# Optimization experiments

Measured on AMD Instinct MI355X. Metric: run time of the kernel, lower is better.

The kernel has to match this reference:

```python
import jax, jax.numpy as jnp
import numpy as np

N, F_IN, H, C, E = 50000, 512, 128, 64, 800000


def setup_inputs() -> dict:
    key = jax.random.key(0)
    ks = jax.random.split(key, 20)
    stdv = 1.0 / np.sqrt(H)
    std_att = 1.0
    std_att_vec = 1.0 / np.sqrt(3.0)
    u = lambda k, shape, s: jax.random.uniform(k, shape, jnp.float32, -s, s)
    inp = {
        "x": jax.random.normal(ks[0], (N, F_IN), jnp.float32),
        "edge_row": jax.random.randint(ks[1], (E,), 0, N, jnp.int32),
        "edge_col": jax.random.randint(ks[2], (E,), 0, N, jnp.int32),
        "edge_val": jax.random.uniform(ks[3], (E,), jnp.float32) * (1.0 / 16.0),
        "weight_low": u(ks[4], (F_IN, H), stdv),
        "weight_high": u(ks[5], (F_IN, H), stdv),
        "weight_mlp": u(ks[6], (F_IN, H), stdv),
        "att_vec_low": u(ks[7], (H, 1), std_att),
        "att_vec_high": u(ks[8], (H, 1), std_att),
        "att_vec_mlp": u(ks[9], (H, 1), std_att),
        "att_vec": u(ks[10], (3, 3), std_att_vec),
        "weight_low2": u(ks[11], (H, C), stdv),
        "weight_high2": u(ks[12], (H, C), stdv),
        "weight_mlp2": u(ks[13], (H, C), stdv),
        "att_vec_low2": u(ks[14], (C, 1), std_att),
        "att_vec_high2": u(ks[15], (C, 1), std_att),
        "att_vec_mlp2": u(ks[16], (C, 1), std_att),
        "att_vec2": u(ks[17], (3, 3), std_att_vec),
    }
    return inp


def _spmm_low(row, col, val, X):
    # adj_low @ X via gather + segment-sum over edges
    return jax.ops.segment_sum(val[:, None] * X[col], row, num_segments=N)


def _attention(o_low, o_high, o_mlp, a_low, a_high, a_mlp, a_vec):
    T = 3.0
    feats = jnp.concatenate([o_low @ a_low, o_high @ a_high, o_mlp @ a_mlp], axis=1)  # [N,3]
    att = jax.nn.softmax(jax.nn.sigmoid(feats) @ a_vec / T, axis=1)
    return att[:, 0:1], att[:, 1:2], att[:, 2:3]


def _layer(X, row, col, val, W_l, W_h, W_m, a_l, a_h, a_m, a_vec):
    xl = X @ W_l
    xh = X @ W_h
    o_low = jax.nn.relu(_spmm_low(row, col, val, xl))
    o_high = jax.nn.relu(xh - _spmm_low(row, col, val, xh))  # (I - adj_low) @ xh
    o_mlp = jax.nn.relu(X @ W_m)
    al, ah, am = _attention(o_low, o_high, o_mlp, a_l, a_h, a_m, a_vec)
    return 3.0 * (al * o_low + ah * o_high + am * o_mlp)


def reference(x, edge_row, edge_col, edge_val, weight_low, weight_high, weight_mlp,
              att_vec_low, att_vec_high, att_vec_mlp, att_vec,
              weight_low2, weight_high2, weight_mlp2,
              att_vec_low2, att_vec_high2, att_vec_mlp2, att_vec2):
    h = _layer(x, edge_row, edge_col, edge_val, weight_low, weight_high, weight_mlp,
               att_vec_low, att_vec_high, att_vec_mlp, att_vec)
    out = _layer(h, edge_row, edge_col, edge_val, weight_low2, weight_high2, weight_mlp2,
                 att_vec_low2, att_vec_high2, att_vec_mlp2, att_vec2)
    return jax.nn.log_softmax(out, axis=1)
```

## Files before the change

### kernel.cpp

```cpp
#include <hip/hip_runtime.h>
#include <hip/hip_bf16.h>

#define NN 50000
#define F_IN 512
#define HH 128
#define CC 64

typedef __attribute__((ext_vector_type(8))) short short8v;
typedef __attribute__((ext_vector_type(4))) float f32x4;
typedef __attribute__((ext_vector_type(2))) float f32x2;

__device__ __forceinline__ short f2b(float f) {
    unsigned u = __builtin_bit_cast(unsigned, f);
    unsigned r = (u + 0x7fffu + ((u >> 16) & 1u)) >> 16;
    return (short)r;
}
__device__ __forceinline__ float b2f(short s) {
    unsigned u = ((unsigned)(unsigned short)s) << 16;
    return __builtin_bit_cast(float, u);
}
__device__ __forceinline__ float b2f_lo(unsigned p) {
    return __builtin_bit_cast(float, p << 16);
}
__device__ __forceinline__ float b2f_hi(unsigned p) {
    return __builtin_bit_cast(float, p & 0xffff0000u);
}

__device__ __forceinline__ f32x2 q2_lo(unsigned p) {
    return __builtin_amdgcn_cvt_pk_f32_fp8(p, false);
}
__device__ __forceinline__ f32x2 q2_hi(unsigned p) {
    return __builtin_amdgcn_cvt_pk_f32_fp8(p, true);
}

__device__ __forceinline__ int xcd_swz(int bid, int nwg) {
    int q = nwg >> 3, r = nwg & 7;
    int xcd = bid & 7, off = bid >> 3;
    return (xcd < r ? xcd * (q + 1) : r * (q + 1) + (xcd - r) * q) + off;
}

__device__ __forceinline__ void load_lds16(const short* g, short* l) {
    __builtin_amdgcn_global_load_lds(
        (const __attribute__((address_space(1))) unsigned int*)g,
        (__attribute__((address_space(3))) unsigned int*)l,
        16, 0, 0);
}

template <int K, int OUTW>
__device__ __forceinline__ void wprep_body(const float* __restrict__ W0,
                                           const float* __restrict__ W1,
                                           const float* __restrict__ W2,
                                           short* __restrict__ Bt, int id) {
    const int nth = 3 * OUTW * (K / 8);
    if (id >= nth) return;
    const int n = id / (K / 8);
    const int kq = id % (K / 8);
    const int sel = n / OUTW;
    const int c = n % OUTW;
    const float* W = sel == 0 ? W0 : (sel == 1 ? W1 : W2);
    short v[8];
#pragma unroll
    for (int j = 0; j < 8; ++j) v[j] = f2b(W[(size_t)(kq * 8 + j) * OUTW + c]);
#pragma unroll
    for (int j = 0; j < 8; ++j) Bt[(size_t)n * K + kq * 8 + j] = v[j];
}

__global__ __launch_bounds__(256) void prep0(int* __restrict__ counts, int n,
                                             const float* __restrict__ Wl,
                                             const float* __restrict__ Wh,
                                             const float* __restrict__ Wm,
                                             short* __restrict__ Bt1,
                                             const float* __restrict__ Wl2,
                                             const float* __restrict__ Wh2,
                                             const float* __restrict__ Wm2,
                                             short* __restrict__ Bt2,
                                             int nZero, int nW1) {
    const int b = blockIdx.x;
    if (b < nZero) {
        int i = b * 256 + threadIdx.x;
        if (i < n) counts[i] = 0;
    } else if (b < nZero + nW1) {
        wprep_body<F_IN, HH>(Wl, Wh, Wm, Bt1, (b - nZero) * 256 + threadIdx.x);
    } else {
        wprep_body<HH, CC>(Wl2, Wh2, Wm2, Bt2, (b - nZero - nW1) * 256 + threadIdx.x);
    }
}

__global__ __launch_bounds__(256) void hist_xconv(const int* __restrict__ erow,
                                                  int* __restrict__ counts, int E,
                                                  const float* __restrict__ x,
                                                  short* __restrict__ xb, int n8,
                                                  int nHist) {
    const int b = blockIdx.x;
    const int total = gridDim.x;
    const long hb4 = ((long)b * nHist) / total;
    const long ha4 = ((long)(b + 1) * nHist) / total;
    if (ha4 != hb4) {
        int i = (int)hb4 * 256 + threadIdx.x;
        if (i < E) atomicAdd(&counts[erow[i]], 1);
        return;
    }
    int i = (b - (int)hb4) * 256 + threadIdx.x;
    if (i >= n8) return;
    const float4* xp = (const float4*)x;
    const float4 a = xp[2 * i];
    const float4 bb = xp[2 * i + 1];
    short8v o;
    o[0] = f2b(a.x); o[1] = f2b(a.y); o[2] = f2b(a.z); o[3] = f2b(a.w);
    o[4] = f2b(bb.x); o[5] = f2b(bb.y); o[6] = f2b(bb.z); o[7] = f2b(bb.w);
    *reinterpret_cast<short8v*>(&xb[(size_t)i * 8]) = o;
}

template <int K, int BNout>
__global__ __launch_bounds__(256) void gemm_scatter(const short* __restrict__ A,
                                                    const short* __restrict__ Bt,
                                                    short* __restrict__ xlh,
                                                    short* __restrict__ xm,
                                                    int M, int nGemm,
                                                    const int* __restrict__ row,
                                                    const int* __restrict__ col,
                                                    const float* __restrict__ val,
                                                    int* __restrict__ cursor,
                                                    int2* __restrict__ edges, int E,
                                                    int nScat) {
    constexpr int BM = 128, BK = 64;
    constexpr int FM = (BNout == 128) ? 4 : 2;
    constexpr int FN = 4;
    constexpr int WM = FM * 16;
    constexpr int NKT = K / BK;
    constexpr int NBL = BNout / 32;

    __shared__ short As[BM * BK];
    __shared__ short Bs[BNout * BK];

    const int total = nGemm + nScat;
    const int swz = xcd_swz(blockIdx.x, total);
    const long ns_b = ((long)swz * nScat) / total;
    const long ns_a = ((long)(swz + 1) * nScat) / total;

    if (ns_a != ns_b) {
        int i = (int)ns_b * 256 + threadIdx.x;
        if (i < E) {
            int r = row[i];
            int p = atomicAdd(&cursor[r], 1);
            int2 rec;
            rec.x = col[i];
            rec.y = __builtin_bit_cast(int, val[i]);
            edges[p] = rec;
        }
        return;
    }

    const int tid = threadIdx.x;
    const int lane = tid & 63;
    const int wid = tid >> 6;
    const int wg = swz - (int)ns_b;
    const int bm = wg / 3;
    const int bn = wg % 3;
    const int m0 = bm * BM;
    const int n0 = bn * BNout;
    const int wm = (BNout == 128) ? (wid >> 1) : wid;
    const int wn = (BNout == 128) ? (wid & 1) : 0;

    const int r8 = lane >> 3;
    const int sl = (lane & 7) ^ r8;

    f32x4 acc[FM][FN];
#pragma unroll
    for (int i = 0; i < FM; ++i)
#pragma unroll
        for (int j = 0; j < FN; ++j) acc[i][j] = (f32x4){0.f, 0.f, 0.f, 0.f};

    for (int kt = 0; kt < NKT; ++kt) {
        const int k0 = kt * BK;
        __syncthreads();
#pragma unroll
        for (int i = 0; i < 4; ++i) {
            int r = (wid * 4 + i) * 8 + r8;
            int gr = m0 + r; if (gr >= M) gr = M - 1;
            load_lds16(&A[(size_t)gr * K + k0 + sl * 8], &As[(wid * 4 + i) * 512]);
        }
#pragma unroll
        for (int i = 0; i < NBL; ++i) {
            int r = (wid * NBL + i) * 8 + r8;
            load_lds16(&Bt[(size_t)(n0 + r) * K + k0 + sl * 8],
                       &Bs[(wid * NBL + i) * 512]);
        }
        __syncthreads();

        const int mrow = lane & 15;
        const int kg = lane >> 4;
#pragma unroll
        for (int kk = 0; kk < 2; ++kk) {
            short8v af[FM], bf[FN];
#pragma unroll
            for (int f = 0; f < FM; ++f) {
                int m = wm * WM + f * 16 + mrow;
                int s = kk * 4 + kg;
                af[f] = *reinterpret_cast<const short8v*>(
                    &As[m * 64 + ((s ^ (m & 7)) << 3)]);
            }
#pragma unroll
            for (int f = 0; f < FN; ++f) {
                int nr = wn * 64 + f * 16 + mrow;
                int s = kk * 4 + kg;
                bf[f] = *reinterpret_cast<const short8v*>(
                    &Bs[nr * 64 + ((s ^ (nr & 7)) << 3)]);
            }
#pragma unroll
            for (int i = 0; i < FM; ++i)
#pragma unroll
                for (int j = 0; j < FN; ++j)
                    acc[i][j] = __builtin_amdgcn_mfma_f32_16x16x32_bf16(
                        af[i], bf[j], acc[i][j], 0, 0, 0);
        }
    }

#pragma unroll
    for (int i = 0; i < FM; ++i)
#pragma unroll
        for (int j = 0; j < FN; ++j) {
            int cc = wn * 64 + j * 16 + (lane & 15);
#pragma unroll
            for (int e = 0; e < 4; ++e) {
                int rrow = m0 + wm * WM + i * 16 + (lane >> 4) * 4 + e;
                if (rrow >= M) continue;
                short v = f2b(acc[i][j][e]);
                if (bn == 2) {
                    xm[(size_t)rrow * BNout + cc] = v;
                } else if (BNout == 128) {
                    xlh[(size_t)rrow * 256 + (cc >> 1) * 4 + bn * 2 + (cc & 1)] = v;
                } else {
                    xlh[(size_t)rrow * 128 + cc * 2 + bn] = v;
                }
            }
        }
}

template <int K, int BNout>
__global__ __launch_bounds__(256) void gemm_mfma(const short* __restrict__ A,
                                                 const short* __restrict__ Bt,
                                                 short* __restrict__ xlh,
                                                 short* __restrict__ xm,
                                                 int M) {
    constexpr int BM = 128, BK = 64;
    constexpr int FM = (BNout == 128) ? 4 : 2;
    constexpr int FN = 4;
    constexpr int WM = FM * 16;
    constexpr int NKT = K / BK;
    constexpr int NBL = BNout / 32;

    __shared__ short As[BM * BK];
    __shared__ short Bs[BNout * BK];

    const int tid = threadIdx.x;
    const int lane = tid & 63;
    const int wid = tid >> 6;
    const int wg = xcd_swz(blockIdx.x, gridDim.x);
    const int bm = wg / 3;
    const int bn = wg % 3;
    const int m0 = bm * BM;
    const int n0 = bn * BNout;
    const int wm = (BNout == 128) ? (wid >> 1) : wid;
    const int wn = (BNout == 128) ? (wid & 1) : 0;

    const int r8 = lane >> 3;
    const int sl = (lane & 7) ^ r8;

    f32x4 acc[FM][FN];
#pragma unroll
    for (int i = 0; i < FM; ++i)
#pragma unroll
        for (int j = 0; j < FN; ++j) acc[i][j] = (f32x4){0.f, 0.f, 0.f, 0.f};

    for (int kt = 0; kt < NKT; ++kt) {
        const int k0 = kt * BK;
        __syncthreads();
#pragma unroll
        for (int i = 0; i < 4; ++i) {
            int r = (wid * 4 + i) * 8 + r8;
            int gr = m0 + r; if (gr >= M) gr = M - 1;
            load_lds16(&A[(size_t)gr * K + k0 + sl * 8], &As[(wid * 4 + i) * 512]);
        }
#pragma unroll
        for (int i = 0; i < NBL; ++i) {
            int r = (wid * NBL + i) * 8 + r8;
            load_lds16(&Bt[(size_t)(n0 + r) * K + k0 + sl * 8],
                       &Bs[(wid * NBL + i) * 512]);
        }
        __syncthreads();

        const int mrow = lane & 15;
        const int kg = lane >> 4;
#pragma unroll
        for (int kk = 0; kk < 2; ++kk) {
            short8v af[FM], bf[FN];
#pragma unroll
            for (int f = 0; f < FM; ++f) {
                int m = wm * WM + f * 16 + mrow;
                int s = kk * 4 + kg;
                af[f] = *reinterpret_cast<const short8v*>(
                    &As[m * 64 + ((s ^ (m & 7)) << 3)]);
            }
#pragma unroll
            for (int f = 0; f < FN; ++f) {
                int nr = wn * 64 + f * 16 + mrow;
                int s = kk * 4 + kg;
                bf[f] = *reinterpret_cast<const short8v*>(
                    &Bs[nr * 64 + ((s ^ (nr & 7)) << 3)]);
            }
#pragma unroll
            for (int i = 0; i < FM; ++i)
#pragma unroll
                for (int j = 0; j < FN; ++j)
                    acc[i][j] = __builtin_amdgcn_mfma_f32_16x16x32_bf16(
                        af[i], bf[j], acc[i][j], 0, 0, 0);
        }
    }

#pragma unroll
    for (int i = 0; i < FM; ++i)
#pragma unroll
        for (int j = 0; j < FN; ++j) {
            int cc = wn * 64 + j * 16 + (lane & 15);
#pragma unroll
            for (int e = 0; e < 4; ++e) {
                int row = m0 + wm * WM + i * 16 + (lane >> 4) * 4 + e;
                if (row >= M) continue;
                short v = f2b(acc[i][j][e]);
                if (bn == 2) {
                    xm[(size_t)row * BNout + cc] = v;
                } else if (BNout == 128) {
                    xlh[(size_t)row * 256 + (cc >> 1) * 4 + bn * 2 + (cc & 1)] = v;
                } else {
                    xlh[(size_t)row * 128 + cc * 2 + bn] = v;
                }
            }
        }
}

__global__ __launch_bounds__(256) void pack8_1(const unsigned* __restrict__ xlh,
                                               unsigned* __restrict__ xq, int n) {
    int i = blockIdx.x * 256 + threadIdx.x;
    if (i >= n) return;
    const uint2 v = ((const uint2*)xlh)[i];
    unsigned r = __builtin_amdgcn_cvt_pk_fp8_f32(b2f_lo(v.x), b2f_hi(v.x), 0, false);
    r = __builtin_amdgcn_cvt_pk_fp8_f32(b2f_lo(v.y), b2f_hi(v.y), r, true);
    xq[i] = r;
}

__global__ __launch_bounds__(256) void pack8_2(const unsigned* __restrict__ xlh,
                                               unsigned* __restrict__ xq, int n2) {
    int i = blockIdx.x * 256 + threadIdx.x;
    if (i >= n2) return;
    const uint2 v = ((const uint2*)xlh)[i];
    unsigned lo = __builtin_amdgcn_cvt_pk_fp8_f32(b2f_lo(v.x), b2f_hi(v.x), 0, false);
    unsigned hi = __builtin_amdgcn_cvt_pk_fp8_f32(b2f_lo(v.y), b2f_hi(v.y), 0, false);
    xq[i] = (lo & 0xffffu) | (hi << 16);
}

__global__ __launch_bounds__(256) void block_sums_kernel(const int* __restrict__ counts,
                                                         int* __restrict__ bsums, int n) {
    __shared__ int s[256];
    int tid = threadIdx.x;
    int i = blockIdx.x * 256 + tid;
    s[tid] = (i < n) ? counts[i] : 0;
    __syncthreads();
#pragma unroll
    for (int off = 128; off > 0; off >>= 1) {
        if (tid < off) s[tid] += s[tid + off];
        __syncthreads();
    }
    if (tid == 0) bsums[blockIdx.x] = s[0];
}

__global__ __launch_bounds__(256) void scan_bsums_kernel(int* __restrict__ bsums, int nb) {
    __shared__ int s[256];
    int t = threadIdx.x;
    int v = (t < nb) ? bsums[t] : 0;
    s[t] = v;
    __syncthreads();
#pragma unroll
    for (int off = 1; off < 256; off <<= 1) {
        int u = (t >= off) ? s[t - off] : 0;
        __syncthreads();
        s[t] += u;
        __syncthreads();
    }
    if (t < nb) bsums[t] = s[t] - v;
}

__global__ __launch_bounds__(256) void scan_final_kernel(const int* __restrict__ counts,
                                                         const int* __restrict__ bsums,
                                                         int* __restrict__ rowptr,
                                                         int* __restrict__ cursor, int n) {
    __shared__ int s[256];
    int tid = threadIdx.x;
    int i = blockIdx.x * 256 + tid;
    int v = (i < n) ? counts[i] : 0;
    s[tid] = v;
    __syncthreads();
#pragma unroll
    for (int off = 1; off < 256; off <<= 1) {
        int t = (tid >= off) ? s[tid - off] : 0;
        __syncthreads();
        s[tid] += t;
        __syncthreads();
    }
    int excl = s[tid] - v + bsums[blockIdx.x];
    if (i < n) {
        rowptr[i] = excl;
        cursor[i] = excl;
        if (i == n - 1) rowptr[n] = excl + v;
    }
}

__device__ __forceinline__ float wave_sum(float v) {
#pragma unroll
    for (int off = 32; off > 0; off >>= 1) v += __shfl_xor(v, off, 64);
    return v;
}
__device__ __forceinline__ float wave_max(float v) {
#pragma unroll
    for (int off = 32; off > 0; off >>= 1) v = fmaxf(v, __shfl_xor(v, off, 64));
    return v;
}

__global__ __launch_bounds__(256) void spmm_att1(const int* __restrict__ rowptr,
                                                 const int2* __restrict__ edges,
                                                 const unsigned* __restrict__ xq,
                                                 const short* __restrict__ xlh,
                                                 const short* __restrict__ xm,
                                                 const float* __restrict__ a_low,
                                                 const float* __restrict__ a_high,
                                                 const float* __restrict__ a_mlp,
                                                 const float* __restrict__ av,
                                                 short* __restrict__ hb,
                                                 int n) {
    const int node = blockIdx.x * 4 + (threadIdx.x >> 6);
    const int lane = threadIdx.x & 63;
    if (node >= n) return;
    const uint2* XLH = (const uint2*)xlh;
    const unsigned* XM = (const unsigned*)xm;

    const int s = __builtin_amdgcn_readfirstlane(rowptr[node]);
    const int e = __builtin_amdgcn_readfirstlane(rowptr[node + 1]);

    float l0 = 0.f, l1 = 0.f, h0 = 0.f, h1 = 0.f;
    for (int j = s; j < e; j += 8) {
        int   cq[8];
        float vq[8];
#pragma unroll
        for (int q = 0; q < 8; ++q) {
            const int jj = min(j + q, e - 1);
            const int2 rec = edges[jj];
            cq[q] = __builtin_amdgcn_readfirstlane(rec.x);
            int vb = __builtin_amdgcn_readfirstlane(rec.y);
            float t = __builtin_bit_cast(float, vb);
            vq[q] = (j + q < e) ? t : 0.f;
        }
        unsigned p[8];
#pragma unroll
        for (int q = 0; q < 8; ++q)
            p[q] = xq[(size_t)cq[q] * 64 + lane];
#pragma unroll
        for (int q = 0; q < 8; ++q) {
            const f32x2 lo = q2_lo(p[q]);
            const f32x2 hi = q2_hi(p[q]);
            l0 += vq[q] * lo.x; l1 += vq[q] * lo.y;
            h0 += vq[q] * hi.x; h1 += vq[q] * hi.y;
        }
    }

    const uint2 self = XLH[(size_t)node * 64 + lane];
    const unsigned xmn = XM[(size_t)node * 64 + lane];
    float ol0 = fmaxf(l0, 0.f);
    float ol1 = fmaxf(l1, 0.f);
    float oh0 = fmaxf(b2f_lo(self.y) - h0, 0.f);
    float oh1 = fmaxf(b2f_hi(self.y) - h1, 0.f);
    float om0 = fmaxf(b2f_lo(xmn), 0.f);
    float om1 = fmaxf(b2f_hi(xmn), 0.f);

    const float2 aL = ((const float2*)a_low)[lane];
    const float2 aH = ((const float2*)a_high)[lane];
    const float2 aM = ((const float2*)a_mlp)[lane];
    float dl = wave_sum(ol0 * aL.x + ol1 * aL.y);
    float dh = wave_sum(oh0 * aH.x + oh1 * aH.y);
    float dm = wave_sum(om0 * aM.x + om1 * aM.y);

    const float g0 = 1.f / (1.f + expf(-dl));
    const float g1 = 1.f / (1.f + expf(-dh));
    const float g2 = 1.f / (1.f + expf(-dm));
    float s0 = (g0 * av[0] + g1 * av[3] + g2 * av[6]) * (1.f / 3.f);
    float s1 = (g0 * av[1] + g1 * av[4] + g2 * av[7]) * (1.f / 3.f);
    float s2 = (g0 * av[2] + g1 * av[5] + g2 * av[8]) * (1.f / 3.f);
    float mx = fmaxf(s0, fmaxf(s1, s2));
    float e0 = expf(s0 - mx), e1 = expf(s1 - mx), e2 = expf(s2 - mx);
    float inv = 1.f / (e0 + e1 + e2);
    float at0 = e0 * inv, at1 = e1 * inv, at2 = e2 * inv;

    float ho0 = 3.f * (at0 * ol0 + at1 * oh0 + at2 * om0);
    float ho1 = 3.f * (at0 * ol1 + at1 * oh1 + at2 * om1);
    unsigned pk = (unsigned)(unsigned short)f2b(ho0) |
                  ((unsigned)(unsigned short)f2b(ho1) << 16);
    ((unsigned*)hb)[(size_t)node * 64 + lane] = pk;
}

__global__ __launch_bounds__(256) void spmm_att2(const int* __restrict__ rowptr,
                                                 const int2* __restrict__ edges,
                                                 const unsigned short* __restrict__ xq,
                                                 const short* __restrict__ xlh,
                                                 const short* __restrict__ xm,
                                                 const float* __restrict__ a_low,
                                                 const float* __restrict__ a_high,
                                                 const float* __restrict__ a_mlp,
                                                 const float* __restrict__ av,
                                                 float* __restrict__ out,
                                                 int n) {
    const int node = blockIdx.x * 4 + (threadIdx.x >> 6);
    const int lane = threadIdx.x & 63;
    if (node >= n) return;
    const unsigned* XLH = (const unsigned*)xlh;

    const int s = __builtin_amdgcn_readfirstlane(rowptr[node]);
    const int e = __builtin_amdgcn_readfirstlane(rowptr[node + 1]);

    float accl = 0.f, acch = 0.f;
    for (int j = s; j < e; j += 8) {
        int   cq[8];
        float vq[8];
#pragma unroll
        for (int q = 0; q < 8; ++q) {
            const int jj = min(j + q, e - 1);
            const int2 rec = edges[jj];
            cq[q] = __builtin_amdgcn_readfirstlane(rec.x);
            int vb = __builtin_amdgcn_readfirstlane(rec.y);
            float t = __builtin_bit_cast(float, vb);
            vq[q] = (j + q < e) ? t : 0.f;
        }
        unsigned short p[8];
#pragma unroll
        for (int q = 0; q < 8; ++q)
            p[q] = xq[(size_t)cq[q] * 64 + lane];
#pragma unroll
        for (int q = 0; q < 8; ++q) {
            const f32x2 d = q2_lo((unsigned)p[q]);
            accl += vq[q] * d.x;
            acch += vq[q] * d.y;
        }
    }

    const unsigned self = XLH[(size_t)node * 64 + lane];
    float ol = fmaxf(accl, 0.f);
    float oh = fmaxf(b2f_hi(self) - acch, 0.f);
    float om = fmaxf(b2f(xm[(size_t)node * 64 + lane]), 0.f);

    float dl = wave_sum(ol * a_low[lane]);
    float dh = wave_sum(oh * a_high[lane]);
    float dm = wave_sum(om * a_mlp[lane]);

    const float g0 = 1.f / (1.f + expf(-dl));
    const float g1 = 1.f / (1.f + expf(-dh));
    const float g2 = 1.f / (1.f + expf(-dm));
    float s0 = (g0 * av[0] + g1 * av[3] + g2 * av[6]) * (1.f / 3.f);
    float s1 = (g0 * av[1] + g1 * av[4] + g2 * av[7]) * (1.f / 3.f);
    float s2 = (g0 * av[2] + g1 * av[5] + g2 * av[8]) * (1.f / 3.f);
    float mx3 = fmaxf(s0, fmaxf(s1, s2));
    float e0 = expf(s0 - mx3), e1 = expf(s1 - mx3), e2 = expf(s2 - mx3);
    float inv = 1.f / (e0 + e1 + e2);
    float at0 = e0 * inv, at1 = e1 * inv, at2 = e2 * inv;

    float o = 3.f * (at0 * ol + at1 * oh + at2 * om);

    float m = wave_max(o);
    float ex = expf(o - m);
    float su = wave_sum(ex);
    out[(size_t)node * 64 + lane] = o - m - logf(su);
}

extern "C" void kernel_launch(void* const* d_in, const int* in_sizes, int n_in,
                              void* d_out, int out_size, void* d_ws, size_t ws_size,
                              hipStream_t stream) {
    const float* x    = (const float*)d_in[0];
    const int*   erow = (const int*)d_in[1];
    const int*   ecol = (const int*)d_in[2];
    const float* eval = (const float*)d_in[3];
    const float* Wl   = (const float*)d_in[4];
    const float* Wh   = (const float*)d_in[5];
    const float* Wm   = (const float*)d_in[6];
    const float* al   = (const float*)d_in[7];
    const float* ah   = (const float*)d_in[8];
    const float* am   = (const float*)d_in[9];
    const float* av   = (const float*)d_in[10];
    const float* Wl2  = (const float*)d_in[11];
    const float* Wh2  = (const float*)d_in[12];
    const float* Wm2  = (const float*)d_in[13];
    const float* al2  = (const float*)d_in[14];
    const float* ah2  = (const float*)d_in[15];
    const float* am2  = (const float*)d_in[16];
    const float* av2  = (const float*)d_in[17];
    float* out = (float*)d_out;

    const int E = in_sizes[1];
    const int N = NN;

    short* ws    = (short*)d_ws;
    short* xb    = ws;
    short* xlh1  = xb + (size_t)N * 512;
    short* xm1   = xlh1 + (size_t)N * 256;
    short* hb    = xm1 + (size_t)N * 128;
    short* Bt1   = hb + (size_t)N * 128;
    short* Bt2   = Bt1 + 384 * 512;
    int*   ip    = (int*)(Bt2 + 192 * 128);
    int*   counts = ip;
    int*   rowptr = ip + N;
    int*   cursor = ip + 2 * N + 1;
    int*   bsums  = ip + 3 * N + 1;
    int2*  edges  = (int2*)(((size_t)(ip + 3 * N + 1 + 256) + 15) & ~(size_t)15);

    unsigned* xq1 = (unsigned*)xb;
    unsigned short* xq2 = (unsigned short*)(xb + (size_t)N * 128);

    short* xlh2 = xlh1;
    short* xm2  = xm1;

    const int NB = (N + 255) / 256;
    const int EB = (E + 255) / 256;
    const int node_blocks = (N + 3) / 4;
    const int MT = (N + 127) / 128;
    const int XCB = (N * F_IN / 8 + 255) / 256;
    const int W1B = (3 * HH * (F_IN / 8) + 255) / 256;
    const int W2B = (3 * CC * (HH / 8) + 255) / 256;
    const int nGemm1 = MT * 3;

    prep0<<<NB + W1B + W2B, 256, 0, stream>>>(counts, N, Wl, Wh, Wm, Bt1,
                                              Wl2, Wh2, Wm2, Bt2, NB, W1B);
    hist_xconv<<<EB + XCB, 256, 0, stream>>>(erow, counts, E, x, xb,
                                             N * F_IN / 8, EB);
    block_sums_kernel<<<NB, 256, 0, stream>>>(counts, bsums, N);
    scan_bsums_kernel<<<1, 256, 0, stream>>>(bsums, NB);
    scan_final_kernel<<<NB, 256, 0, stream>>>(counts, bsums, rowptr, cursor, N);

    gemm_scatter<F_IN, HH><<<nGemm1 + EB, 256, 0, stream>>>(
        xb, Bt1, xlh1, xm1, N, nGemm1, erow, ecol, eval, cursor, edges, E, EB);
    pack8_1<<<(N * 64 + 255) / 256, 256, 0, stream>>>((const unsigned*)xlh1, xq1, N * 64);
    spmm_att1<<<node_blocks, 256, 0, stream>>>(rowptr, edges,
                                               xq1, xlh1, xm1, al, ah, am, av, hb, N);

    gemm_mfma<HH, CC><<<MT * 3, 256, 0, stream>>>(hb, Bt2, xlh2, xm2, N);
    pack8_2<<<(N * 32 + 255) / 256, 256, 0, stream>>>((const unsigned*)xlh2,
                                                      (unsigned*)xq2, N * 32);
    spmm_att2<<<node_blocks, 256, 0, stream>>>(rowptr, edges,
                                               xq2, xlh2, xm2, al2, ah2, am2, av2, out, N);
}
```

Measured before the change: 224.9 us.

## Stage GEMM output tiles through LDS and store separate planar xl/xh/xm buffers

The GEMM epilogue previously wrote scattered 2-byte stores into an interleaved low/high layout. Now the bf16 tile goes to shared memory first and is written out with coalesced 16-byte stores into separate xl, xh and xm planes. The pack kernels and SpMM kernels are changed to read the planar buffers. This cuts uncoalesced global writes at the cost of an extra LDS round trip and barriers, and the self-term reads in the SpMM kernels now come from a different plane.

```diff
diff --git a/kernel.cpp b/kernel.cpp
--- a/kernel.cpp
+++ b/kernel.cpp
@@ -112,9 +112,119 @@
 }
 
 template <int K, int BNout>
+__device__ __forceinline__ void gemm_body(const short* __restrict__ A,
+                                          const short* __restrict__ Bt,
+                                          short* __restrict__ xl,
+                                          short* __restrict__ xh,
+                                          short* __restrict__ xm,
+                                          int M, int wg, short* smem) {
+    constexpr int BM = 128, BK = 64;
+    constexpr int FM = (BNout == 128) ? 4 : 2;
+    constexpr int FN = 4;
+    constexpr int WM = FM * 16;
+    constexpr int NKT = K / BK;
+    constexpr int NBL = BNout / 32;
+
+    short* As = smem;
+    short* Bs = smem + BM * BK;
+
+    const int tid = threadIdx.x;
+    const int lane = tid & 63;
+    const int wid = tid >> 6;
+    const int bm = wg / 3;
+    const int bn = wg % 3;
+    const int m0 = bm * BM;
+    const int n0 = bn * BNout;
+    const int wm = (BNout == 128) ? (wid >> 1) : wid;
+    const int wn = (BNout == 128) ? (wid & 1) : 0;
+
+    const int r8 = lane >> 3;
+    const int sl = (lane & 7) ^ r8;
+
+    f32x4 acc[FM][FN];
+#pragma unroll
+    for (int i = 0; i < FM; ++i)
+#pragma unroll
+        for (int j = 0; j < FN; ++j) acc[i][j] = (f32x4){0.f, 0.f, 0.f, 0.f};
+
+    for (int kt = 0; kt < NKT; ++kt) {
+        const int k0 = kt * BK;
+        __syncthreads();
+#pragma unroll
+        for (int i = 0; i < 4; ++i) {
+            int r = (wid * 4 + i) * 8 + r8;
+            int gr = m0 + r; if (gr >= M) gr = M - 1;
+            load_lds16(&A[(size_t)gr * K + k0 + sl * 8], &As[(wid * 4 + i) * 512]);
+        }
+#pragma unroll
+        for (int i = 0; i < NBL; ++i) {
+            int r = (wid * NBL + i) * 8 + r8;
+            load_lds16(&Bt[(size_t)(n0 + r) * K + k0 + sl * 8],
+                       &Bs[(wid * NBL + i) * 512]);
+        }
+        __syncthreads();
+
+        const int mrow = lane & 15;
+        const int kg = lane >> 4;
+#pragma unroll
+        for (int kk = 0; kk < 2; ++kk) {
+            short8v af[FM], bf[FN];
+#pragma unroll
+            for (int f = 0; f < FM; ++f) {
+                int m = wm * WM + f * 16 + mrow;
+                int s = kk * 4 + kg;
+                af[f] = *reinterpret_cast<const short8v*>(
+                    &As[m * 64 + ((s ^ (m & 7)) << 3)]);
+            }
+#pragma unroll
+            for (int f = 0; f < FN; ++f) {
+                int nr = wn * 64 + f * 16 + mrow;
+                int s = kk * 4 + kg;
+                bf[f] = *reinterpret_cast<const short8v*>(
+                    &Bs[nr * 64 + ((s ^ (nr & 7)) << 3)]);
+            }
+#pragma unroll
+            for (int i = 0; i < FM; ++i)
+#pragma unroll
+                for (int j = 0; j < FN; ++j)
+                    acc[i][j] = __builtin_amdgcn_mfma_f32_16x16x32_bf16(
+                        af[i], bf[j], acc[i][j], 0, 0, 0);
+        }
+    }
+
+    __syncthreads();
+#pragma unroll
+    for (int i = 0; i < FM; ++i)
+#pragma unroll
+        for (int j = 0; j < FN; ++j) {
+            int cc = wn * 64 + j * 16 + (lane & 15);
+#pragma unroll
+            for (int e = 0; e < 4; ++e) {
+                int r = wm * WM + i * 16 + (lane >> 4) * 4 + e;
+                smem[r * BNout + cc] = f2b(acc[i][j][e]);
+            }
+        }
+    __syncthreads();
+
+    short* plane = (bn == 0) ? xl : ((bn == 1) ? xh : xm);
+    constexpr int CH = BM * BNout / 8;
+#pragma unroll
+    for (int p = 0; p < CH / 256; ++p) {
+        int idx = p * 256 + tid;
+        int r = idx / (BNout / 8);
+        int c8 = idx % (BNout / 8);
+        int grow = m0 + r;
+        if (grow < M)
+            *reinterpret_cast<int4*>(&plane[(size_t)grow * BNout + c8 * 8]) =
+                *reinterpret_cast<const int4*>(&smem[r * BNout + c8 * 8]);
+    }
+}
+
+template <int K, int BNout>
 __global__ __launch_bounds__(256) void gemm_scatter(const short* __restrict__ A,
                                                     const short* __restrict__ Bt,
-                                                    short* __restrict__ xlh,
+                                                    short* __restrict__ xl,
+                                                    short* __restrict__ xh,
                                                     short* __restrict__ xm,
                                                     int M, int nGemm,
                                                     const int* __restrict__ row,
@@ -123,15 +233,7 @@
                                                     int* __restrict__ cursor,
                                                     int2* __restrict__ edges, int E,
                                                     int nScat) {
-    constexpr int BM = 128, BK = 64;
-    constexpr int FM = (BNout == 128) ? 4 : 2;
-    constexpr int FN = 4;
-    constexpr int WM = FM * 16;
-    constexpr int NKT = K / BK;
-    constexpr int NBL = BNout / 32;
-
-    __shared__ short As[BM * BK];
-    __shared__ short Bs[BNout * BK];
+    __shared__ short smem[128 * 64 + BNout * 64];
 
     const int total = nGemm + nScat;
     const int swz = xcd_swz(blockIdx.x, total);
@@ -150,213 +252,42 @@
         }
         return;
     }
-
-    const int tid = threadIdx.x;
-    const int lane = tid & 63;
-    const int wid = tid >> 6;
-    const int wg = swz - (int)ns_b;
-    const int bm = wg / 3;
-    const int bn = wg % 3;
-    const int m0 = bm * BM;
-    const int n0 = bn * BNout;
-    const int wm = (BNout == 128) ? (wid >> 1) : wid;
-    const int wn = (BNout == 128) ? (wid & 1) : 0;
-
-    const int r8 = lane >> 3;
-    const int sl = (lane & 7) ^ r8;
-
-    f32x4 acc[FM][FN];
-#pragma unroll
-    for (int i = 0; i < FM; ++i)
-#pragma unroll
-        for (int j = 0; j < FN; ++j) acc[i][j] = (f32x4){0.f, 0.f, 0.f, 0.f};
-
-    for (int kt = 0; kt < NKT; ++kt) {
-        const int k0 = kt * BK;
-        __syncthreads();
-#pragma unroll
-        for (int i = 0; i < 4; ++i) {
-            int r = (wid * 4 + i) * 8 + r8;
-            int gr = m0 + r; if (gr >= M) gr = M - 1;
-            load_lds16(&A[(size_t)gr * K + k0 + sl * 8], &As[(wid * 4 + i) * 512]);
-        }
-#pragma unroll
-        for (int i = 0; i < NBL; ++i) {
-            int r = (wid * NBL + i) * 8 + r8;
-            load_lds16(&Bt[(size_t)(n0 + r) * K + k0 + sl * 8],
-                       &Bs[(wid * NBL + i) * 512]);
-        }
-        __syncthreads();
-
-        const int mrow = lane & 15;
-        const int kg = lane >> 4;
-#pragma unroll
-        for (int kk = 0; kk < 2; ++kk) {
-            short8v af[FM], bf[FN];
-#pragma unroll
-            for (int f = 0; f < FM; ++f) {
-                int m = wm * WM + f * 16 + mrow;
-                int s = kk * 4 + kg;
-                af[f] = *reinterpret_cast<const short8v*>(
-                    &As[m * 64 + ((s ^ (m & 7)) << 3)]);
-            }
-#pragma unroll
-            for (int f = 0; f < FN; ++f) {
-                int nr = wn * 64 + f * 16 + mrow;
-                int s = kk * 4 + kg;
-                bf[f] = *reinterpret_cast<const short8v*>(
-                    &Bs[nr * 64 + ((s ^ (nr & 7)) << 3)]);
-            }
-#pragma unroll
-            for (int i = 0; i < FM; ++i)
-#pragma unroll
-                for (int j = 0; j < FN; ++j)
-                    acc[i][j] = __builtin_amdgcn_mfma_f32_16x16x32_bf16(
-                        af[i], bf[j], acc[i][j], 0, 0, 0);
-        }
-    }
-
-#pragma unroll
-    for (int i = 0; i < FM; ++i)
-#pragma unroll
-        for (int j = 0; j < FN; ++j) {
-            int cc = wn * 64 + j * 16 + (lane & 15);
-#pragma unroll
-            for (int e = 0; e < 4; ++e) {
-                int rrow = m0 + wm * WM + i * 16 + (lane >> 4) * 4 + e;
-                if (rrow >= M) continue;
-                short v = f2b(acc[i][j][e]);
-                if (bn == 2) {
-                    xm[(size_t)rrow * BNout + cc] = v;
-                } else if (BNout == 128) {
-                    xlh[(size_t)rrow * 256 + (cc >> 1) * 4 + bn * 2 + (cc & 1)] = v;
-                } else {
-                    xlh[(size_t)rrow * 128 + cc * 2 + bn] = v;
-                }
-            }
-        }
+    gemm_body<K, BNout>(A, Bt, xl, xh, xm, M, swz - (int)ns_b, smem);
 }
 
 template <int K, int BNout>
 __global__ __launch_bounds__(256) void gemm_mfma(const short* __restrict__ A,
                                                  const short* __restrict__ Bt,
-                                                 short* __restrict__ xlh,
+                                                 short* __restrict__ xl,
+                                                 short* __restrict__ xh,
                                                  short* __restrict__ xm,
                                                  int M) {
-    constexpr int BM = 128, BK = 64;
-    constexpr int FM = (BNout == 128) ? 4 : 2;
-    constexpr int FN = 4;
-    constexpr int WM = FM * 16;
-    constexpr int NKT = K / BK;
-    constexpr int NBL = BNout / 32;
-
-    __shared__ short As[BM * BK];
-    __shared__ short Bs[BNout * BK];
-
-    const int tid = threadIdx.x;
-    const int lane = tid & 63;
-    const int wid = tid >> 6;
-    const int wg = xcd_swz(blockIdx.x, gridDim.x);
-    const int bm = wg / 3;
-    const int bn = wg % 3;
-    const int m0 = bm * BM;
-    const int n0 = bn * BNout;
-    const int wm = (BNout == 128) ? (wid >> 1) : wid;
-    const int wn = (BNout == 128) ? (wid & 1) : 0;
-
-    const int r8 = lane >> 3;
-    const int sl = (lane & 7) ^ r8;
-
-    f32x4 acc[FM][FN];
-#pragma unroll
-    for (int i = 0; i < FM; ++i)
-#pragma unroll
-        for (int j = 0; j < FN; ++j) acc[i][j] = (f32x4){0.f, 0.f, 0.f, 0.f};
-
-    for (int kt = 0; kt < NKT; ++kt) {
-        const int k0 = kt * BK;
-        __syncthreads();
-#pragma unroll
-        for (int i = 0; i < 4; ++i) {
-            int r = (wid * 4 + i) * 8 + r8;
-            int gr = m0 + r; if (gr >= M) gr = M - 1;
-            load_lds16(&A[(size_t)gr * K + k0 + sl * 8], &As[(wid * 4 + i) * 512]);
-        }
-#pragma unroll
-        for (int i = 0; i < NBL; ++i) {
-            int r = (wid * NBL + i) * 8 + r8;
-            load_lds16(&Bt[(size_t)(n0 + r) * K + k0 + sl * 8],
-                       &Bs[(wid * NBL + i) * 512]);
-        }
-        __syncthreads();
-
-        const int mrow = lane & 15;
-        const int kg = lane >> 4;
-#pragma unroll
-        for (int kk = 0; kk < 2; ++kk) {
-            short8v af[FM], bf[FN];
-#pragma unroll
-            for (int f = 0; f < FM; ++f) {
-                int m = wm * WM + f * 16 + mrow;
-                int s = kk * 4 + kg;
-                af[f] = *reinterpret_cast<const short8v*>(
-                    &As[m * 64 + ((s ^ (m & 7)) << 3)]);
-            }
-#pragma unroll
-            for (int f = 0; f < FN; ++f) {
-                int nr = wn * 64 + f * 16 + mrow;
-                int s = kk * 4 + kg;
-                bf[f] = *reinterpret_cast<const short8v*>(
-                    &Bs[nr * 64 + ((s ^ (nr & 7)) << 3)]);
-            }
-#pragma unroll
-            for (int i = 0; i < FM; ++i)
-#pragma unroll
-                for (int j = 0; j < FN; ++j)
-                    acc[i][j] = __builtin_amdgcn_mfma_f32_16x16x32_bf16(
-                        af[i], bf[j], acc[i][j], 0, 0, 0);
-        }
-    }
-
-#pragma unroll
-    for (int i = 0; i < FM; ++i)
-#pragma unroll
-        for (int j = 0; j < FN; ++j) {
-            int cc = wn * 64 + j * 16 + (lane & 15);
-#pragma unroll
-            for (int e = 0; e < 4; ++e) {
-                int row = m0 + wm * WM + i * 16 + (lane >> 4) * 4 + e;
-                if (row >= M) continue;
-                short v = f2b(acc[i][j][e]);
-                if (bn == 2) {
-                    xm[(size_t)row * BNout + cc] = v;
-                } else if (BNout == 128) {
-                    xlh[(size_t)row * 256 + (cc >> 1) * 4 + bn * 2 + (cc & 1)] = v;
-                } else {
-                    xlh[(size_t)row * 128 + cc * 2 + bn] = v;
-                }
-            }
-        }
-}
-
-__global__ __launch_bounds__(256) void pack8_1(const unsigned* __restrict__ xlh,
+    __shared__ short smem[128 * 64 + BNout * 64];
+    gemm_body<K, BNout>(A, Bt, xl, xh, xm, M, xcd_swz(blockIdx.x, gridDim.x), smem);
+}
+
+__global__ __launch_bounds__(256) void pack8_1(const unsigned* __restrict__ xl,
+                                               const unsigned* __restrict__ xh,
                                                unsigned* __restrict__ xq, int n) {
     int i = blockIdx.x * 256 + threadIdx.x;
     if (i >= n) return;
-    const uint2 v = ((const uint2*)xlh)[i];
-    unsigned r = __builtin_amdgcn_cvt_pk_fp8_f32(b2f_lo(v.x), b2f_hi(v.x), 0, false);
-    r = __builtin_amdgcn_cvt_pk_fp8_f32(b2f_lo(v.y), b2f_hi(v.y), r, true);
+    const unsigned vx = xl[i];
+    const unsigned vh = xh[i];
+    unsigned r = __builtin_amdgcn_cvt_pk_fp8_f32(b2f_lo(vx), b2f_hi(vx), 0, false);
+    r = __builtin_amdgcn_cvt_pk_fp8_f32(b2f_lo(vh), b2f_hi(vh), r, true);
     xq[i] = r;
 }
 
-__global__ __launch_bounds__(256) void pack8_2(const unsigned* __restrict__ xlh,
-                                               unsigned* __restrict__ xq, int n2) {
+__global__ __launch_bounds__(256) void pack8_2(const unsigned* __restrict__ xl,
+                                               const unsigned* __restrict__ xh,
+                                               unsigned* __restrict__ xq, int n) {
     int i = blockIdx.x * 256 + threadIdx.x;
-    if (i >= n2) return;
-    const uint2 v = ((const uint2*)xlh)[i];
-    unsigned lo = __builtin_amdgcn_cvt_pk_fp8_f32(b2f_lo(v.x), b2f_hi(v.x), 0, false);
-    unsigned hi = __builtin_amdgcn_cvt_pk_fp8_f32(b2f_lo(v.y), b2f_hi(v.y), 0, false);
-    xq[i] = (lo & 0xffffu) | (hi << 16);
+    if (i >= n) return;
+    const unsigned vx = xl[i];
+    const unsigned vh = xh[i];
+    unsigned r = __builtin_amdgcn_cvt_pk_fp8_f32(b2f_lo(vx), b2f_lo(vh), 0, false);
+    r = __builtin_amdgcn_cvt_pk_fp8_f32(b2f_hi(vx), b2f_hi(vh), r, true);
+    xq[i] = r;
 }
 
 __global__ __launch_bounds__(256) void block_sums_kernel(const int* __restrict__ counts,
@@ -429,8 +360,8 @@
 __global__ __launch_bounds__(256) void spmm_att1(const int* __restrict__ rowptr,
                                                  const int2* __restrict__ edges,
                                                  const unsigned* __restrict__ xq,
-                                                 const short* __restrict__ xlh,
-                                                 const short* __restrict__ xm,
+                                                 const unsigned* __restrict__ xhp,
+                                                 const unsigned* __restrict__ xmp,
                                                  const float* __restrict__ a_low,
                                                  const float* __restrict__ a_high,
                                                  const float* __restrict__ a_mlp,
@@ -440,8 +371,6 @@
     const int node = blockIdx.x * 4 + (threadIdx.x >> 6);
     const int lane = threadIdx.x & 63;
     if (node >= n) return;
-    const uint2* XLH = (const uint2*)xlh;
-    const unsigned* XM = (const unsigned*)xm;
 
     const int s = __builtin_amdgcn_readfirstlane(rowptr[node]);
     const int e = __builtin_amdgcn_readfirstlane(rowptr[node + 1]);
@@ -472,12 +401,12 @@
         }
     }
 
-    const uint2 self = XLH[(size_t)node * 64 + lane];
-    const unsigned xmn = XM[(size_t)node * 64 + lane];
+    const unsigned xhn = xhp[(size_t)node * 64 + lane];
+    const unsigned xmn = xmp[(size_t)node * 64 + lane];
     float ol0 = fmaxf(l0, 0.f);
     float ol1 = fmaxf(l1, 0.f);
-    float oh0 = fmaxf(b2f_lo(self.y) - h0, 0.f);
-    float oh1 = fmaxf(b2f_hi(self.y) - h1, 0.f);
+    float oh0 = fmaxf(b2f_lo(xhn) - h0, 0.f);
+    float oh1 = fmaxf(b2f_hi(xhn) - h1, 0.f);
     float om0 = fmaxf(b2f_lo(xmn), 0.f);
     float om1 = fmaxf(b2f_hi(xmn), 0.f);
 
@@ -509,8 +438,8 @@
 __global__ __launch_bounds__(256) void spmm_att2(const int* __restrict__ rowptr,
                                                  const int2* __restrict__ edges,
                                                  const unsigned short* __restrict__ xq,
-                                                 const short* __restrict__ xlh,
-                                                 const short* __restrict__ xm,
+                                                 const short* __restrict__ xhp,
+                                                 const short* __restrict__ xmp,
                                                  const float* __restrict__ a_low,
                                                  const float* __restrict__ a_high,
                                                  const float* __restrict__ a_mlp,
@@ -520,7 +449,6 @@
     const int node = blockIdx.x * 4 + (threadIdx.x >> 6);
     const int lane = threadIdx.x & 63;
     if (node >= n) return;
-    const unsigned* XLH = (const unsigned*)xlh;
 
     const int s = __builtin_amdgcn_readfirstlane(rowptr[node]);
     const int e = __builtin_amdgcn_readfirstlane(rowptr[node + 1]);
@@ -550,10 +478,9 @@
         }
     }
 
-    const unsigned self = XLH[(size_t)node * 64 + lane];
     float ol = fmaxf(accl, 0.f);
-    float oh = fmaxf(b2f_hi(self) - acch, 0.f);
-    float om = fmaxf(b2f(xm[(size_t)node * 64 + lane]), 0.f);
+    float oh = fmaxf(b2f(xhp[(size_t)node * 64 + lane]) - acch, 0.f);
+    float om = fmaxf(b2f(xmp[(size_t)node * 64 + lane]), 0.f);
 
     float dl = wave_sum(ol * a_low[lane]);
     float dh = wave_sum(oh * a_high[lane]);
@@ -606,8 +533,9 @@
 
     short* ws    = (short*)d_ws;
     short* xb    = ws;
-    short* xlh1  = xb + (size_t)N * 512;
-    short* xm1   = xlh1 + (size_t)N * 256;
+    short* xl1   = xb + (size_t)N * 512;
+    short* xh1   = xl1 + (size_t)N * 128;
+    short* xm1   = xh1 + (size_t)N * 128;
     short* hb    = xm1 + (size_t)N * 128;
     short* Bt1   = hb + (size_t)N * 128;
     short* Bt2   = Bt1 + 384 * 512;
@@ -621,8 +549,9 @@
     unsigned* xq1 = (unsigned*)xb;
     unsigned short* xq2 = (unsigned short*)(xb + (size_t)N * 128);
 
-    short* xlh2 = xlh1;
-    short* xm2  = xm1;
+    short* xl2 = xl1;
+    short* xh2 = xl1 + (size_t)N * 64;
+    short* xm2 = xl1 + (size_t)N * 128;
 
     const int NB = (N + 255) / 256;
     const int EB = (E + 255) / 256;
@@ -642,14 +571,18 @@
     scan_final_kernel<<<NB, 256, 0, stream>>>(counts, bsums, rowptr, cursor, N);
 
     gemm_scatter<F_IN, HH><<<nGemm1 + EB, 256, 0, stream>>>(
-        xb, Bt1, xlh1, xm1, N, nGemm1, erow, ecol, eval, cursor, edges, E, EB);
-    pack8_1<<<(N * 64 + 255) / 256, 256, 0, stream>>>((const unsigned*)xlh1, xq1, N * 64);
-    spmm_att1<<<node_blocks, 256, 0, stream>>>(rowptr, edges,
-                                               xq1, xlh1, xm1, al, ah, am, av, hb, N);
-
-    gemm_mfma<HH, CC><<<MT * 3, 256, 0, stream>>>(hb, Bt2, xlh2, xm2, N);
-    pack8_2<<<(N * 32 + 255) / 256, 256, 0, stream>>>((const unsigned*)xlh2,
+        xb, Bt1, xl1, xh1, xm1, N, nGemm1, erow, ecol, eval, cursor, edges, E, EB);
+    pack8_1<<<(N * 64 + 255) / 256, 256, 0, stream>>>((const unsigned*)xl1,
+                                                      (const unsigned*)xh1, xq1, N * 64);
+    spmm_att1<<<node_blocks, 256, 0, stream>>>(rowptr, edges, xq1,
+                                               (const unsigned*)xh1,
+                                               (const unsigned*)xm1,
+                                               al, ah, am, av, hb, N);
+
+    gemm_mfma<HH, CC><<<MT * 3, 256, 0, stream>>>(hb, Bt2, xl2, xh2, xm2, N);
+    pack8_2<<<(N * 32 + 255) / 256, 256, 0, stream>>>((const unsigned*)xl2,
+                                                      (const unsigned*)xh2,
                                                       (unsigned*)xq2, N * 32);
-    spmm_att2<<<node_blocks, 256, 0, stream>>>(rowptr, edges,
-                                               xq2, xlh2, xm2, al2, ah2, am2, av2, out, N);
-}
+    spmm_att2<<<node_blocks, 256, 0, stream>>>(rowptr, edges, xq2, xh2, xm2,
+                                               al2, ah2, am2, av2, out, N);
+}
```

After: 206.1 us. -8.4%, faster.
